# Performance work log

Measured on AMD Instinct MI355X. Metric: run time of the kernel, lower is better.

The kernel has to match this reference:

```python
import jax, jax.numpy as jnp
import numpy as np


def conv2d(x, w, b=None, pad=0):
    # x: [B,C,H,W], w: [O,I,kh,kw]
    out = jax.lax.conv_general_dilated(
        x, w, window_strides=(1, 1), padding=[(pad, pad), (pad, pad)],
        dimension_numbers=('NCHW', 'OIHW', 'NCHW'))
    if b is not None:
        out = out + b[None, :, None, None]
    return out


def setup_inputs() -> dict:
    key = jax.random.key(0)
    ks = jax.random.split(key, 10)
    B, C, W, H, N, G = 8, 256, 64, 64, 1024, 32
    s = jnp.float32(0.02)  # small init so softmax is not saturated
    return {
        'input_graph': jax.random.normal(ks[0], (B, N, G), jnp.float32),
        'input_image': jax.random.normal(ks[1], (B, C, W, H), jnp.float32),
        'Wq': jax.random.normal(ks[2], (C, C), jnp.float32) * s,
        'bq': jnp.zeros((C,), jnp.float32),
        'Wk': jax.random.normal(ks[3], (C, G), jnp.float32) * s,
        'bk': jnp.zeros((C,), jnp.float32),
        'Wv': jax.random.normal(ks[4], (C, G), jnp.float32) * s,
        'bv': jnp.zeros((C,), jnp.float32),
        'conv1_w': jax.random.normal(ks[5], (C, C, 1, 1), jnp.float32) * s,
        'bn_gamma': jnp.ones((C,), jnp.float32),
        'bn_beta': jnp.zeros((C,), jnp.float32),
        'bn_mean': jnp.zeros((C,), jnp.float32),
        'bn_var': jnp.ones((C,), jnp.float32),
        'conv2_w': jax.random.normal(ks[6], (C, C, 3, 3), jnp.float32) * s,
        'conv2_b': jnp.zeros((C,), jnp.float32),
        'conv3_w': jax.random.normal(ks[7], (C, C, 1, 1), jnp.float32) * s,
        'conv3_b': jnp.zeros((C,), jnp.float32),
    }


def reference(input_graph, input_image, Wq, bq, Wk, bk, Wv, bv,
              conv1_w, bn_gamma, bn_beta, bn_mean, bn_var,
              conv2_w, conv2_b, conv3_w, conv3_b):
    B, C, W, H = input_image.shape
    P = W * H
    g = jnp.transpose(input_graph, (0, 2, 1))  # [B,G,N]
    # 1x1 conv1d projections == per-position matmuls
    K = jnp.einsum('og,bgn->bon', Wk, g) + bk[None, :, None]   # [B,C,N]
    V = jnp.einsum('og,bgn->bon', Wv, g) + bv[None, :, None]   # [B,C,N]
    x = input_image.reshape(B, C, P)
    Q = jnp.einsum('oc,bcp->bop', Wq, x) + bq[None, :, None]   # [B,C,P]
    # att[b,p,n] = sum_c Q[b,c,p] * K[b,c,n]  (Q was permuted to [B,P,C] in torch)
    att = jnp.einsum('bcp,bcn->bpn', Q, K) / jnp.sqrt(jnp.float32(C))
    # NOTE: original applies Softmax(dim=1) -> over the P (pixel) axis
    att = jax.nn.softmax(att, axis=1)
    # message = V @ att^T : [B,C,N] x [B,N,P] -> [B,C,P]
    msg = jnp.einsum('bcn,bpn->bcp', V, att).reshape(B, C, W, H)
    # Conv_Bn_Activation: 1x1 conv (no bias) + BN (inference) + LeakyReLU(0.1)
    h = conv2d(msg, conv1_w)
    inv = jax.lax.rsqrt(bn_var + jnp.float32(1e-5))
    h = (h - bn_mean[None, :, None, None]) * (bn_gamma * inv)[None, :, None, None] + bn_beta[None, :, None, None]
    h = jnp.where(h > 0, h, jnp.float32(0.1) * h)
    h = conv2d(h, conv2_w, conv2_b, pad=1)  # 3x3, pad 1
    return input_image + conv2d(h, conv3_w, conv3_b)  # 1x1
```

## Files before the change

### kernel.cpp

```cpp
#include <hip/hip_runtime.h>
#include <hip/hip_bf16.h>

typedef __hip_bfloat16 bf16;
typedef unsigned short u16;
typedef __attribute__((ext_vector_type(8))) short  b8v;
typedef __attribute__((ext_vector_type(8))) unsigned short u16x8;
typedef __attribute__((ext_vector_type(4))) unsigned short u16x4;
typedef __attribute__((ext_vector_type(4))) float f32x4;

static __device__ __forceinline__ float us2f(u16 s) {
    unsigned int u = ((unsigned int)s) << 16;
    return __builtin_bit_cast(float, u);
}
static __device__ __forceinline__ u16 f2us(float x) {
    union { bf16 h; u16 s; } v; v.h = __float2bfloat16(x); return v.s;
}
static __device__ __forceinline__ float b2f(bf16 x) { return __bfloat162float(x); }
static __device__ __forceinline__ bf16 f2b(float x) { return __float2bfloat16(x); }
static __device__ __forceinline__ float toF(float x) { return x; }
static __device__ __forceinline__ float toF(bf16 x)  { return b2f(x); }
static __device__ __forceinline__ void stor(float* p, float v) { *p = v; }
static __device__ __forceinline__ void stor(bf16* p,  float v) { *p = f2b(v); }

static __device__ __forceinline__ void gload16(const u16* g, u16* l) {
    __builtin_amdgcn_global_load_lds(
        (const __attribute__((address_space(1))) unsigned int*)g,
        (__attribute__((address_space(3))) unsigned int*)l,
        16, 0, 0);
}


__global__ __launch_bounds__(256) void cast_f2b4(const float* __restrict__ src,
                                                 u16* __restrict__ dst, int n4)
{
    int i = blockIdx.x * 256 + threadIdx.x;
    if (i < n4) {
        float4 v = ((const float4*)src)[i];
        u16x4 o = { f2us(v.x), f2us(v.y), f2us(v.z), f2us(v.w) };
        ((u16x4*)dst)[i] = o;
    }
}

__global__ __launch_bounds__(256) void repack_w2(const float* __restrict__ src,
                                                 u16* __restrict__ dst)
{
    int idx = blockIdx.x * 256 + threadIdx.x;
    int o = idx / 2304, k = idx - o * 2304;
    int tap = k >> 8, c = k & 255;
    dst[idx] = f2us(src[(o * 256 + c) * 9 + tap]);
}

__global__ __launch_bounds__(256) void transpose_cast_x(const float* __restrict__ x,
                                                        u16* __restrict__ xT, int C, int P)
{
    __shared__ u16 t[64][72];
    const int b = blockIdx.z, c0 = blockIdx.y * 64, p0 = blockIdx.x * 64;
    const int tid = threadIdx.x;
    const int r = tid >> 2, q = tid & 3;
    const float* src = x + ((size_t)b * C + c0 + r) * P + p0 + q * 16;
#pragma unroll
    for (int i = 0; i < 16; i++) t[q * 16 + i][r] = f2us(src[i]);
    __syncthreads();
    u16* dst = xT + ((size_t)b * P + p0 + r) * C + c0 + q * 16;
    *(u16x8*)dst       = *(u16x8*)&t[r][q * 16];
    *(u16x8*)(dst + 8) = *(u16x8*)&t[r][q * 16 + 8];
}

__global__ __launch_bounds__(256) void fold_k(const float* __restrict__ Wk,
                                              const float* __restrict__ Wq,
                                              const float* __restrict__ bk,
                                              const float* __restrict__ bq,
                                              float* __restrict__ WkWq, float* __restrict__ kqb,
                                              float* __restrict__ wkbq, float* __restrict__ bqbk)
{
    const int g = blockIdx.x;
    const int c = threadIdx.x;
    float s = 0.f;
#pragma unroll 8
    for (int o = 0; o < 256; o++) s += Wk[o * 32 + g] * Wq[o * 256 + c];
    WkWq[g * 256 + c] = s;
    if (blockIdx.x == 0) {
        float t = 0.f;
#pragma unroll 8
        for (int o = 0; o < 256; o++) t += bk[o] * Wq[o * 256 + c];
        kqb[c] = t;
    }
    if (threadIdx.x == 0) {
        float u = 0.f;
#pragma unroll 8
        for (int o = 0; o < 256; o++) u += bq[o] * Wk[o * 32 + g];
        wkbq[g] = u;
    }
    if (blockIdx.x == 0 && threadIdx.x == 1) {
        float u = 0.f;
#pragma unroll 8
        for (int o = 0; o < 256; o++) u += bq[o] * bk[o];
        bqbk[0] = u;
    }
}

__global__ __launch_bounds__(64) void fold_v(const float* __restrict__ c1w,
                                             const float* __restrict__ Wv,
                                             const float* __restrict__ bv,
                                             float* __restrict__ W1V, float* __restrict__ b1v)
{
    const int o = blockIdx.x;
    const int g = threadIdx.x;
    if (g < 32) {
        float s = 0.f;
#pragma unroll 8
        for (int c = 0; c < 256; c++) s += c1w[o * 256 + c] * Wv[c * 32 + g];
        W1V[o * 32 + g] = s;
    } else if (g == 32) {
        float s = 0.f;
#pragma unroll 8
        for (int c = 0; c < 256; c++) s += c1w[o * 256 + c] * bv[c];
        b1v[o] = s;
    }
}

__global__ __launch_bounds__(256) void tq_small(const float* __restrict__ graph,
                                                const float* __restrict__ wkbq,
                                                const float* __restrict__ bqbk,
                                                float* __restrict__ tq, int N, int G)
{
    const int n = blockIdx.x * 256 + threadIdx.x, b = blockIdx.y;
    const float* row = graph + ((size_t)b * N + n) * G;
    float s = bqbk[0];
#pragma unroll
    for (int g = 0; g < 32; g++) s += row[g] * wkbq[g];
    tq[(size_t)b * N + n] = s;
}

template<int EPI, typename TA, typename TB, typename TC>
__global__ __launch_bounds__(256) void gemm_any(
    const TA* __restrict__ A, const TB* __restrict__ B, TC* __restrict__ C,
    int M, int Nn, int Kd,
    long saM, long saK, long aB,
    long sbK, long sbN, long bB,
    long scM, long scN, long cB,
    float scale, const float* __restrict__ bias, const float* __restrict__ scl)
{
    __shared__ float As[16][65];
    __shared__ float Bs[16][65];
    const int b  = blockIdx.z;
    const TA* Ab = A + (long)b * aB;
    const TB* Bb = B + (long)b * bB;
    const int m0 = blockIdx.y * 64, n0 = blockIdx.x * 64;
    const int tid = threadIdx.x;
    const int tx = tid & 15, ty = tid >> 4;
    const bool kfA = (saK == 1);
    const bool nfB = (sbN == 1);
    float acc[4][4] = {};

    for (int k0 = 0; k0 < Kd; k0 += 16) {
#pragma unroll
        for (int i = 0; i < 4; i++) {
            int idx = tid + i * 256; int mm, kk;
            if (kfA) { kk = idx & 15; mm = idx >> 4; }
            else     { mm = idx & 63; kk = idx >> 6; }
            As[kk][mm] = toF(Ab[(long)(m0 + mm) * saM + (long)(k0 + kk) * saK]);
        }
#pragma unroll
        for (int i = 0; i < 4; i++) {
            int idx = tid + i * 256; int nn, kk;
            if (nfB) { nn = idx & 63; kk = idx >> 6; }
            else     { kk = idx & 15; nn = idx >> 4; }
            Bs[kk][nn] = toF(Bb[(long)(k0 + kk) * sbK + (long)(n0 + nn) * sbN]);
        }
        __syncthreads();
#pragma unroll
        for (int kk = 0; kk < 16; kk++) {
            float a[4], bb[4];
#pragma unroll
            for (int i = 0; i < 4; i++) a[i]  = As[kk][ty * 4 + i];
#pragma unroll
            for (int j = 0; j < 4; j++) bb[j] = Bs[kk][tx * 4 + j];
#pragma unroll
            for (int i = 0; i < 4; i++)
#pragma unroll
                for (int j = 0; j < 4; j++) acc[i][j] += a[i] * bb[j];
        }
        __syncthreads();
    }
#pragma unroll
    for (int i = 0; i < 4; i++) {
        int m = m0 + ty * 4 + i;
        float add0 = ((EPI == 0 || EPI == 4) && bias) ? bias[m] : 0.f;
#pragma unroll
        for (int j = 0; j < 4; j++) {
            int n = n0 + tx * 4 + j;
            float v = acc[i][j] * scale + add0;
            if (EPI == 3 && bias) v += bias[n];
            if (EPI == 4) v *= scl[(long)b * Nn + n];
            stor(&C[(long)b * cB + (long)m * scM + (long)n * scN], v);
        }
    }
}

template<int EPI, bool CT, typename TC, int NTILE>
__global__ __launch_bounds__(256) void gemm_mfma(
    const u16* __restrict__ A, const u16* __restrict__ Bt, TC* __restrict__ Cc,
    int M, int N, int K, int lda, int ldb, int ldc,
    long aBat, long bBat, long cBat,
    float scale, const float* __restrict__ bias,
    const float* __restrict__ gamma, const float* __restrict__ beta,
    const float* __restrict__ mean,  const float* __restrict__ var,
    const float* __restrict__ resid, long rBat, int ldr,
    float* __restrict__ csum)
{
    constexpr int NI = NTILE / 32;
    __shared__ u16 Al[128 * 32];
    __shared__ u16 Bl[NTILE * 32];
    __shared__ float red[(EPI == 3) ? 256 : 1];
    __shared__ u16 tbuf[(EPI == 3) ? 64 * 136 : 1];
    const int bat = blockIdx.z;
    const int nxy = gridDim.x * gridDim.y;
    const int fid = blockIdx.y * gridDim.x + blockIdx.x;
    const int swzid = (fid & 7) * (nxy >> 3) + (fid >> 3);
    const int bidx = swzid % gridDim.x, bidy = swzid / gridDim.x;
    const int m0 = bidy * 128, n0 = bidx * NTILE;
    const int tid = threadIdx.x;
    const int lane = tid & 63, wid = tid >> 6;
    const int wr = wid >> 1, wc = wid & 1;
    const int fr = lane & 15, fq = lane >> 4;
    const int sc = ((lane & 3) ^ ((lane >> 3) & 3)) * 8;
    const int axs = (fq ^ ((fr >> 1) & 3)) * 8;

    const u16* gA = A  + (size_t)bat * aBat + (size_t)(m0 + wid * 32 + (lane >> 2)) * lda + sc;
    const u16* gB = Bt + (size_t)bat * bBat + (size_t)(n0 + wid * (NTILE / 4) + (lane >> 2)) * ldb + sc;
    u16* lA = &Al[(wid * 32) * 32];
    u16* lB = &Bl[(wid * (NTILE / 4)) * 32];
    const size_t a16 = (size_t)16 * lda, b16 = (size_t)16 * ldb;

    f32x4 acc[4][NI];
#pragma unroll
    for (int i = 0; i < 4; i++)
#pragma unroll
        for (int j = 0; j < NI; j++) acc[i][j] = (f32x4){0.f, 0.f, 0.f, 0.f};

    for (int k0 = 0; k0 < K; k0 += 32) {
        gload16(gA + k0,       lA);
        gload16(gA + k0 + a16, lA + 16 * 32);
        gload16(gB + k0,       lB);
        if constexpr (NTILE == 128) gload16(gB + k0 + b16, lB + 16 * 32);
        __syncthreads();
        b8v a[4], b[NI];
#pragma unroll
        for (int mi = 0; mi < 4; mi++) a[mi] = *(const b8v*)&Al[(wr * 64 + mi * 16 + fr) * 32 + axs];
#pragma unroll
        for (int ni = 0; ni < NI; ni++) b[ni] = *(const b8v*)&Bl[(wc * (NTILE / 2) + ni * 16 + fr) * 32 + axs];
#pragma unroll
        for (int mi = 0; mi < 4; mi++)
#pragma unroll
            for (int ni = 0; ni < NI; ni++)
                acc[mi][ni] = __builtin_amdgcn_mfma_f32_16x16x32_bf16(a[mi], b[ni], acc[mi][ni], 0, 0, 0);
        __syncthreads();
    }

    const int mbase = m0 + wr * 64, nbase = n0 + wc * (NTILE / 2);

    if constexpr (EPI == 3) {
        float cs[NI];
#pragma unroll
        for (int ni = 0; ni < NI; ni++) cs[ni] = 0.f;
#pragma unroll
        for (int h = 0; h < 2; h++) {
#pragma unroll
            for (int mh = 0; mh < 2; mh++) {
                const int mi = h * 2 + mh;
                const int trow = wr * 32 + mh * 16 + fq * 4;
#pragma unroll
                for (int ni = 0; ni < NI; ni++) {
                    const int n = nbase + ni * 16 + fr;
                    const float tqv = bias ? bias[(size_t)bat * N + n] : 0.f;
                    f32x4 v = acc[mi][ni];
#pragma unroll
                    for (int j = 0; j < 4; j++) {
                        float x = __expf((v[j] + tqv) * scale);
                        cs[ni] += x;
                        tbuf[(trow + j) * 136 + wc * 64 + ni * 16 + fr] = f2us(x);
                    }
                }
            }
            __syncthreads();
#pragma unroll
            for (int it = 0; it < 4; it++) {
                const int idx = it * 256 + tid;
                const int row = idx >> 4, ng = idx & 15;
                const int m = m0 + (row >> 5) * 64 + h * 32 + (row & 31);
                u16x8 v8 = *(const u16x8*)&tbuf[row * 136 + ng * 8];
                *(u16x8*)((u16*)Cc + (size_t)bat * cBat + (size_t)m * ldc + n0 + ng * 8) = v8;
            }
            __syncthreads();
        }
#pragma unroll
        for (int ni = 0; ni < NI; ni++) {
            float s = cs[ni];
            s += __shfl_xor(s, 16, 64);
            s += __shfl_xor(s, 32, 64);
            if (fq == 0) red[wr * 128 + wc * 64 + ni * 16 + fr] = s;
        }
        __syncthreads();
        if (tid < NTILE) {
            float s = red[tid] + red[128 + tid];
            csum[((size_t)bat * gridDim.y + bidy) * ldc + n0 + tid] = s;
        }
        return;
    }

#pragma unroll
    for (int mi = 0; mi < 4; mi++) {
        float esc[4], ead[4];
#pragma unroll
        for (int j = 0; j < 4; j++) {
            int m = mbase + mi * 16 + fq * 4 + j;
            if (EPI == 1) {
                float sc2 = gamma[m] * rsqrtf(var[m] + 1e-5f);
                esc[j] = sc2; ead[j] = beta[m] - mean[m] * sc2;
            } else {
                esc[j] = scale;
                ead[j] = 0.f;
            }
        }
#pragma unroll
        for (int ni = 0; ni < NI; ni++) {
            f32x4 v = acc[mi][ni];
            const int n = nbase + ni * 16 + fr;
            if (CT) {
                const int mb = mbase + mi * 16 + fq * 4;
                if constexpr (EPI == 4) {
                    const float bb = bias ? bias[n] : 0.f;
                    float4 rv = *(const float4*)&resid[(size_t)bat * rBat + (size_t)n * ldr + mb];
                    float4 o4;
                    o4.x = v[0] * scale + bb + rv.x;
                    o4.y = v[1] * scale + bb + rv.y;
                    o4.z = v[2] * scale + bb + rv.z;
                    o4.w = v[3] * scale + bb + rv.w;
                    *(float4*)((float*)Cc + (size_t)bat * cBat + (size_t)n * ldc + mb) = o4;
                } else {
                    const long crow = (EPI == 1)
                        ? (long)(((n >> 6) + 1) * 66 + (n & 63) + 1)
                        : (long)n;
                    u16x4 pk;
#pragma unroll
                    for (int j = 0; j < 4; j++) {
                        float x = v[j] * esc[j] + ead[j];
                        if (EPI == 1) x = x > 0.f ? x : 0.1f * x;
                        pk[j] = f2us(x);
                    }
                    *(u16x4*)((u16*)Cc + (size_t)bat * cBat + (size_t)crow * ldc + mb) = pk;
                }
            } else {
#pragma unroll
                for (int j = 0; j < 4; j++) {
                    int m = mbase + mi * 16 + fq * 4 + j;
                    float x = v[j] * esc[j] + ead[j];
                    if (EPI == 1) x = x > 0.f ? x : 0.1f * x;
                    TC* p = Cc + (size_t)bat * cBat + (size_t)m * ldc + n;
                    if constexpr (sizeof(TC) == 2) *(u16*)p = f2us(x); else *(float*)p = x;
                }
            }
        }
    }
}

__global__ __launch_bounds__(256) void conv3x3_mfma(
    const u16* __restrict__ Wt, const u16* __restrict__ Xp, u16* __restrict__ Y,
    const float* __restrict__ bias)
{
    const int C = 256, P = 4096, K = 2304;
    __shared__ u16 Al[2][128 * 32];
    __shared__ u16 Bl[64 * 64];
    const int bat = blockIdx.z;
    const int m0 = blockIdx.y * 128;
    const int y0 = blockIdx.x;
    const int tid = threadIdx.x;
    const int lane = tid & 63, wid = tid >> 6;
    const int wr = wid >> 1, wc = wid & 1;
    const int fr = lane & 15, fq = lane >> 4;
    const int scA = ((lane & 3) ^ ((lane >> 3) & 3)) * 8;
    const int axs = (fq ^ ((fr >> 1) & 3)) * 8;

    const u16* Ag = Wt + (size_t)(m0 + wid * 32 + (lane >> 2)) * K + scA;
    u16* lA0 = &Al[0][(wid * 32) * 32];
    u16* lA1 = &Al[1][(wid * 32) * 32];
    const u16* Xb = Xp + (size_t)bat * 66 * 66 * 256;

    const int brow = (lane >> 3), bq = lane & 7;

    f32x4 acc[4][2];
#pragma unroll
    for (int i = 0; i < 4; i++)
#pragma unroll
        for (int j = 0; j < 2; j++) acc[i][j] = (f32x4){0.f, 0.f, 0.f, 0.f};

    for (int k0 = 0; k0 < K; k0 += 64) {
        const int tap = k0 >> 8, c0k = k0 & 255;
        const int dy = tap / 3 - 1, dxv = tap - (tap / 3) * 3 - 1;
        const int syp = y0 + dy + 1;
        gload16(Ag + k0,                       lA0);
        gload16(Ag + k0 + (size_t)16 * K,      lA0 + 16 * 32);
        gload16(Ag + k0 + 32,                  lA1);
        gload16(Ag + k0 + 32 + (size_t)16 * K, lA1 + 16 * 32);
#pragma unroll
        for (int h = 0; h < 2; h++) {
            const int g = wid * 2 + h;
            const int r = g * 8 + brow;
            const int qs = bq ^ (r & 7);
            const u16* src = Xb + ((size_t)syp * 66 + (r + dxv + 1)) * 256 + c0k + qs * 8;
            gload16(src, &Bl[g * 512]);
        }
        __syncthreads();
#pragma unroll
        for (int t = 0; t < 2; t++) {
            b8v a[4], b[2];
#pragma unroll
            for (int mi = 0; mi < 4; mi++) a[mi] = *(const b8v*)&Al[t][(wr * 64 + mi * 16 + fr) * 32 + axs];
#pragma unroll
            for (int ni = 0; ni < 2; ni++) {
                const int row = wc * 32 + ni * 16 + fr;
                const int ch = ((t * 4 + fq) ^ (row & 7)) * 8;
                b[ni] = *(const b8v*)&Bl[row * 64 + ch];
            }
#pragma unroll
            for (int mi = 0; mi < 4; mi++)
#pragma unroll
                for (int ni = 0; ni < 2; ni++)
                    acc[mi][ni] = __builtin_amdgcn_mfma_f32_16x16x32_bf16(a[mi], b[ni], acc[mi][ni], 0, 0, 0);
        }
        __syncthreads();
    }

    const int mbase = m0 + wr * 64, nbase = y0 * 64 + wc * 32;
#pragma unroll
    for (int mi = 0; mi < 4; mi++) {
        const int mb = mbase + mi * 16 + fq * 4;
        float bb[4];
#pragma unroll
        for (int j = 0; j < 4; j++) bb[j] = bias[mb + j];
#pragma unroll
        for (int ni = 0; ni < 2; ni++) {
            const int n = nbase + ni * 16 + fr;
            u16x4 pk;
#pragma unroll
            for (int j = 0; j < 4; j++) pk[j] = f2us(acc[mi][ni][j] + bb[j]);
            *(u16x4*)&Y[(size_t)bat * P * C + (size_t)n * C + mb] = pk;
        }
    }
}


__global__ __launch_bounds__(256) void colsum_merge(const float* __restrict__ part,
                                                    float* __restrict__ sinv, int N, int PC)
{
    const int n = blockIdx.x * 256 + threadIdx.x, b = blockIdx.y;
    const float* pc = part + (size_t)b * PC * N + n;
    float s = 0.f;
    for (int c = 0; c < PC; c++) s += pc[(size_t)c * N];
    sinv[(size_t)b * N + n] = 1.f / s;
}

__global__ __launch_bounds__(256) void zero_halo(u16* __restrict__ Xp)
{
    int i = blockIdx.x * 256 + threadIdx.x;
    const int ch8 = i & 31; i >>= 5;
    const int hp = i % 260;
    const int b = i / 260;
    int py, px;
    if (hp < 66)       { py = 0;  px = hp; }
    else if (hp < 132) { py = 65; px = hp - 66; }
    else if (hp < 196) { py = hp - 132 + 1; px = 0; }
    else               { py = hp - 196 + 1; px = 65; }
    u16x8 z = {0, 0, 0, 0, 0, 0, 0, 0};
    *(u16x8*)&Xp[(((size_t)b * 66 + py) * 66 + px) * 256 + ch8 * 8] = z;
}


extern "C" void kernel_launch(void* const* d_in, const int* in_sizes, int n_in,
                              void* d_out, int out_size, void* d_ws, size_t ws_size,
                              hipStream_t stream)
{
    const float* graph = (const float*)d_in[0];
    const float* image = (const float*)d_in[1];
    const float* Wq  = (const float*)d_in[2];
    const float* bq  = (const float*)d_in[3];
    const float* Wk  = (const float*)d_in[4];
    const float* bk  = (const float*)d_in[5];
    const float* Wv  = (const float*)d_in[6];
    const float* bv  = (const float*)d_in[7];
    const float* c1w = (const float*)d_in[8];
    const float* gam = (const float*)d_in[9];
    const float* bet = (const float*)d_in[10];
    const float* mea = (const float*)d_in[11];
    const float* var = (const float*)d_in[12];
    const float* c2w = (const float*)d_in[13];
    const float* c2b = (const float*)d_in[14];
    const float* c3w = (const float*)d_in[15];
    const float* c3b = (const float*)d_in[16];
    float* out = (float*)d_out;

    const int B = 8, C = 256, P = 4096, N = 1024, G = 32;
    const size_t MiB = 1024 * 1024, KiB = 1024;
    char* ws = (char*)d_ws;
    char* dob = (char*)d_out;
    u16* E    = (u16*)(ws);
    u16* xT   = (u16*)(ws + 64 * MiB);
    u16* VV   = (u16*)(ws + 80 * MiB);
    u16* h2T  = (u16*)(ws);
    u16* c2w_b = (u16*)(ws + 17 * MiB);
    u16* c3w_b = (u16*)(ws + 19 * MiB);
    float* part = (float*)(dob);
    u16* KWt   = (u16*)(dob + 2 * MiB);
    float* tqb = (float*)(dob + 6 * MiB);
    float* sinv = (float*)(dob + 7 * MiB);
    float* WkWq = (float*)(dob + 8 * MiB);
    float* kqb  = (float*)(dob + 8 * MiB + 64 * KiB);
    float* wkbq = (float*)(dob + 8 * MiB + 128 * KiB);
    float* bqbk = (float*)(dob + 8 * MiB + 160 * KiB);
    float* W1V  = (float*)(dob + 9 * MiB);
    float* b1v  = (float*)(dob + 9 * MiB + 64 * KiB);
    u16* h1p   = (u16*)(dob + 14 * MiB);

    transpose_cast_x<<<dim3(P / 64, C / 64, B), 256, 0, stream>>>(image, xT, C, P);
    fold_k<<<32, 256, 0, stream>>>(Wk, Wq, bk, bq, WkWq, kqb, wkbq, bqbk);
    fold_v<<<256, 64, 0, stream>>>(c1w, Wv, bv, W1V, b1v);
    zero_halo<<<260, 256, 0, stream>>>(h1p);
    gemm_any<3, float, float, bf16><<<dim3(C / 64, N / 64, B), 256, 0, stream>>>(
        graph, WkWq, (bf16*)KWt, N, C, G,
        G, 1, (long)N * G,   C, 1, 0,   C, 1, (long)N * C, 1.f, kqb, nullptr);
    tq_small<<<dim3(N / 256, B), 256, 0, stream>>>(graph, wkbq, bqbk, tqb, N, G);
    gemm_mfma<3, false, u16, 128><<<dim3(N / 128, P / 128, B), 256, 0, stream>>>(
        xT, KWt, E, P, N, C, C, C, N,
        (long)P * C, (long)N * C, (long)P * N, 0.0625f, tqb,
        nullptr, nullptr, nullptr, nullptr, nullptr, 0, 0, part);
    colsum_merge<<<dim3(N / 256, B), 256, 0, stream>>>(part, sinv, N, P / 128);
    gemm_any<4, float, float, bf16><<<dim3(N / 64, C / 64, B), 256, 0, stream>>>(
        W1V, graph, (bf16*)VV, C, N, G,
        G, 1, 0,   1, G, (long)N * G,   N, 1, (long)C * N, 1.f, b1v, sinv);
    gemm_mfma<1, true, u16, 128><<<dim3(P / 128, C / 128, B), 256, 0, stream>>>(
        VV, E, h1p, C, P, N, N, N, C,
        (long)C * N, (long)P * N, (long)66 * 66 * C, 1.f, nullptr,
        gam, bet, mea, var, nullptr, 0, 0, nullptr);
    repack_w2<<<2304, 256, 0, stream>>>(c2w, c2w_b);
    cast_f2b4<<<64, 256, 0, stream>>>(c3w, c3w_b, 16384);
    conv3x3_mfma<<<dim3(P / 64, C / 128, B), 256, 0, stream>>>(c2w_b, h1p, h2T, c2b);
    gemm_mfma<4, true, float, 64><<<dim3(C / 64, P / 128, B), 256, 0, stream>>>(
        h2T, c3w_b, out, P, C, C, C, C, P,
        (long)P * C, 0, (long)C * P, 1.f, c3b,
        nullptr, nullptr, nullptr, nullptr, image, (long)C * P, P, nullptr);
}
```

Measured before the change: 235.0 us.

## Fold 1x1 conv3 into 3x3 conv weights and fuse residual into conv epilogue

Pre-multiplies the conv3 1x1 weights into the conv2 3x3 weights (and folds the biases) so the final 1x1 GEMM and its bf16 intermediate disappear. The conv3x3 kernel now writes fp32 output directly with the residual added. This removes a full GEMM pass and an intermediate write and read, at the cost of a small weight-folding GEMM per call. The epilogue now writes scalar, strided-by-P floats instead of vectorized packed stores, which may hurt store coalescing. Changing the order of rounding through bf16 may also shift numerics slightly.

```diff
diff --git a/kernel.cpp b/kernel.cpp
--- a/kernel.cpp
+++ b/kernel.cpp
@@ -30,17 +30,6 @@
 }
 
 
-__global__ __launch_bounds__(256) void cast_f2b4(const float* __restrict__ src,
-                                                 u16* __restrict__ dst, int n4)
-{
-    int i = blockIdx.x * 256 + threadIdx.x;
-    if (i < n4) {
-        float4 v = ((const float4*)src)[i];
-        u16x4 o = { f2us(v.x), f2us(v.y), f2us(v.z), f2us(v.w) };
-        ((u16x4*)dst)[i] = o;
-    }
-}
-
 __global__ __launch_bounds__(256) void repack_w2(const float* __restrict__ src,
                                                  u16* __restrict__ dst)
 {
@@ -102,7 +91,11 @@
 __global__ __launch_bounds__(64) void fold_v(const float* __restrict__ c1w,
                                              const float* __restrict__ Wv,
                                              const float* __restrict__ bv,
-                                             float* __restrict__ W1V, float* __restrict__ b1v)
+                                             const float* __restrict__ c3w,
+                                             const float* __restrict__ c2b,
+                                             const float* __restrict__ c3b,
+                                             float* __restrict__ W1V, float* __restrict__ b1v,
+                                             float* __restrict__ bfold)
 {
     const int o = blockIdx.x;
     const int g = threadIdx.x;
@@ -116,6 +109,11 @@
 #pragma unroll 8
         for (int c = 0; c < 256; c++) s += c1w[o * 256 + c] * bv[c];
         b1v[o] = s;
+    } else if (g == 33) {
+        float s = 0.f;
+#pragma unroll 8
+        for (int m = 0; m < 256; m++) s += c3w[o * 256 + m] * c2b[m];
+        bfold[o] = s + c3b[o];
     }
 }
 
@@ -206,7 +204,6 @@
     float scale, const float* __restrict__ bias,
     const float* __restrict__ gamma, const float* __restrict__ beta,
     const float* __restrict__ mean,  const float* __restrict__ var,
-    const float* __restrict__ resid, long rBat, int ldr,
     float* __restrict__ csum)
 {
     constexpr int NI = NTILE / 32;
@@ -318,10 +315,7 @@
             if (EPI == 1) {
                 float sc2 = gamma[m] * rsqrtf(var[m] + 1e-5f);
                 esc[j] = sc2; ead[j] = beta[m] - mean[m] * sc2;
-            } else {
-                esc[j] = scale;
-                ead[j] = 0.f;
-            }
+            } else { esc[j] = scale; ead[j] = 0.f; }
         }
 #pragma unroll
         for (int ni = 0; ni < NI; ni++) {
@@ -329,28 +323,17 @@
             const int n = nbase + ni * 16 + fr;
             if (CT) {
                 const int mb = mbase + mi * 16 + fq * 4;
-                if constexpr (EPI == 4) {
-                    const float bb = bias ? bias[n] : 0.f;
-                    float4 rv = *(const float4*)&resid[(size_t)bat * rBat + (size_t)n * ldr + mb];
-                    float4 o4;
-                    o4.x = v[0] * scale + bb + rv.x;
-                    o4.y = v[1] * scale + bb + rv.y;
-                    o4.z = v[2] * scale + bb + rv.z;
-                    o4.w = v[3] * scale + bb + rv.w;
-                    *(float4*)((float*)Cc + (size_t)bat * cBat + (size_t)n * ldc + mb) = o4;
-                } else {
-                    const long crow = (EPI == 1)
-                        ? (long)(((n >> 6) + 1) * 66 + (n & 63) + 1)
-                        : (long)n;
-                    u16x4 pk;
-#pragma unroll
-                    for (int j = 0; j < 4; j++) {
-                        float x = v[j] * esc[j] + ead[j];
-                        if (EPI == 1) x = x > 0.f ? x : 0.1f * x;
-                        pk[j] = f2us(x);
-                    }
-                    *(u16x4*)((u16*)Cc + (size_t)bat * cBat + (size_t)crow * ldc + mb) = pk;
+                const long crow = (EPI == 1)
+                    ? (long)(((n >> 6) + 1) * 66 + (n & 63) + 1)
+                    : (long)n;
+                u16x4 pk;
+#pragma unroll
+                for (int j = 0; j < 4; j++) {
+                    float x = v[j] * esc[j] + ead[j];
+                    if (EPI == 1) x = x > 0.f ? x : 0.1f * x;
+                    pk[j] = f2us(x);
                 }
+                *(u16x4*)((u16*)Cc + (size_t)bat * cBat + (size_t)crow * ldc + mb) = pk;
             } else {
 #pragma unroll
                 for (int j = 0; j < 4; j++) {
@@ -366,7 +349,8 @@
 }
 
 __global__ __launch_bounds__(256) void conv3x3_mfma(
-    const u16* __restrict__ Wt, const u16* __restrict__ Xp, u16* __restrict__ Y,
+    const u16* __restrict__ Wt, const u16* __restrict__ Xp,
+    const float* __restrict__ resid, float* __restrict__ outF,
     const float* __restrict__ bias)
 {
     const int C = 256, P = 4096, K = 2304;
@@ -433,6 +417,7 @@
     }
 
     const int mbase = m0 + wr * 64, nbase = y0 * 64 + wc * 32;
+    const size_t obase = (size_t)bat * C * P;
 #pragma unroll
     for (int mi = 0; mi < 4; mi++) {
         const int mb = mbase + mi * 16 + fq * 4;
@@ -442,10 +427,11 @@
 #pragma unroll
         for (int ni = 0; ni < 2; ni++) {
             const int n = nbase + ni * 16 + fr;
-            u16x4 pk;
-#pragma unroll
-            for (int j = 0; j < 4; j++) pk[j] = f2us(acc[mi][ni][j] + bb[j]);
-            *(u16x4*)&Y[(size_t)bat * P * C + (size_t)n * C + mb] = pk;
+#pragma unroll
+            for (int j = 0; j < 4; j++) {
+                const size_t off = obase + (size_t)(mb + j) * P + n;
+                outF[off] = acc[mi][ni][j] + bb[j] + resid[off];
+            }
         }
     }
 }
@@ -504,12 +490,12 @@
     const size_t MiB = 1024 * 1024, KiB = 1024;
     char* ws = (char*)d_ws;
     char* dob = (char*)d_out;
-    u16* E    = (u16*)(ws);
-    u16* xT   = (u16*)(ws + 64 * MiB);
-    u16* VV   = (u16*)(ws + 80 * MiB);
-    u16* h2T  = (u16*)(ws);
-    u16* c2w_b = (u16*)(ws + 17 * MiB);
-    u16* c3w_b = (u16*)(ws + 19 * MiB);
+    u16* E     = (u16*)(ws);
+    u16* xT    = (u16*)(ws + 64 * MiB);
+    u16* h1p   = (u16*)(ws + 64 * MiB);
+    u16* c2w_b = (u16*)(ws + 81 * MiB + 512 * KiB);
+    float* bfold = (float*)(ws + 83 * MiB);
+    u16* VV    = (u16*)(ws + 84 * MiB);
     float* part = (float*)(dob);
     u16* KWt   = (u16*)(dob + 2 * MiB);
     float* tqb = (float*)(dob + 6 * MiB);
@@ -520,12 +506,15 @@
     float* bqbk = (float*)(dob + 8 * MiB + 160 * KiB);
     float* W1V  = (float*)(dob + 9 * MiB);
     float* b1v  = (float*)(dob + 9 * MiB + 64 * KiB);
-    u16* h1p   = (u16*)(dob + 14 * MiB);
+    float* c2wf = (float*)(dob + 10 * MiB);
 
     transpose_cast_x<<<dim3(P / 64, C / 64, B), 256, 0, stream>>>(image, xT, C, P);
     fold_k<<<32, 256, 0, stream>>>(Wk, Wq, bk, bq, WkWq, kqb, wkbq, bqbk);
-    fold_v<<<256, 64, 0, stream>>>(c1w, Wv, bv, W1V, b1v);
-    zero_halo<<<260, 256, 0, stream>>>(h1p);
+    fold_v<<<256, 64, 0, stream>>>(c1w, Wv, bv, c3w, c2b, c3b, W1V, b1v, bfold);
+    gemm_any<0, float, float, float><<<dim3(2304 / 64, C / 64, 1), 256, 0, stream>>>(
+        c3w, c2w, c2wf, C, 2304, C,
+        C, 1, 0,   2304, 1, 0,   2304, 1, 0, 1.f, nullptr, nullptr);
+    repack_w2<<<2304, 256, 0, stream>>>(c2wf, c2w_b);
     gemm_any<3, float, float, bf16><<<dim3(C / 64, N / 64, B), 256, 0, stream>>>(
         graph, WkWq, (bf16*)KWt, N, C, G,
         G, 1, (long)N * G,   C, 1, 0,   C, 1, (long)N * C, 1.f, kqb, nullptr);
@@ -533,20 +522,16 @@
     gemm_mfma<3, false, u16, 128><<<dim3(N / 128, P / 128, B), 256, 0, stream>>>(
         xT, KWt, E, P, N, C, C, C, N,
         (long)P * C, (long)N * C, (long)P * N, 0.0625f, tqb,
-        nullptr, nullptr, nullptr, nullptr, nullptr, 0, 0, part);
+        nullptr, nullptr, nullptr, nullptr, part);
     colsum_merge<<<dim3(N / 256, B), 256, 0, stream>>>(part, sinv, N, P / 128);
+    zero_halo<<<260, 256, 0, stream>>>(h1p);
     gemm_any<4, float, float, bf16><<<dim3(N / 64, C / 64, B), 256, 0, stream>>>(
         W1V, graph, (bf16*)VV, C, N, G,
         G, 1, 0,   1, G, (long)N * G,   N, 1, (long)C * N, 1.f, b1v, sinv);
     gemm_mfma<1, true, u16, 128><<<dim3(P / 128, C / 128, B), 256, 0, stream>>>(
         VV, E, h1p, C, P, N, N, N, C,
         (long)C * N, (long)P * N, (long)66 * 66 * C, 1.f, nullptr,
-        gam, bet, mea, var, nullptr, 0, 0, nullptr);
-    repack_w2<<<2304, 256, 0, stream>>>(c2w, c2w_b);
-    cast_f2b4<<<64, 256, 0, stream>>>(c3w, c3w_b, 16384);
-    conv3x3_mfma<<<dim3(P / 64, C / 128, B), 256, 0, stream>>>(c2w_b, h1p, h2T, c2b);
-    gemm_mfma<4, true, float, 64><<<dim3(C / 64, P / 128, B), 256, 0, stream>>>(
-        h2T, c3w_b, out, P, C, C, C, C, P,
-        (long)P * C, 0, (long)C * P, 1.f, c3b,
-        nullptr, nullptr, nullptr, nullptr, image, (long)C * P, P, nullptr);
-}
+        gam, bet, mea, var, nullptr);
+    conv3x3_mfma<<<dim3(P / 64, C / 128, B), 256, 0, stream>>>(
+        c2w_b, h1p, image, out, bfold);
+}
```

After: 261.9 us. 11.4% more time.
